# Performance work log

Hardware: AMD Instinct MI355X
Metric: run time of the kernel (lower is better)

Reference implementation:

```python
import jax, jax.numpy as jnp
import numpy as np

EPS = 1e-5  # batch-norm epsilon


def subm_conv(feat, nbrs, W):
    # feat: [N, Cin], nbrs: [N, K] int indices into feat (rulebook), W: [K, Cin, Cout]
    gathered = feat[nbrs]                      # [N, K, Cin]  irregular gather
    return jnp.einsum('nkc,kcd->nd', gathered, W)


def batch_norm(f, gamma, beta):
    # training-mode BN over active sites (scn.BatchNormalization semantics)
    mean = jnp.mean(f, axis=0)
    var = jnp.var(f, axis=0)
    return (f - mean) * jax.lax.rsqrt(var + EPS) * gamma + beta


def setup_inputs() -> dict:
    key = jax.random.key(0)
    k1, k2, k3, k4 = jax.random.split(key, 4)
    N, K, C = 300000, 9, 64
    scale = 1.0 / np.sqrt(K * C)
    return {
        'x': jax.random.normal(k1, (N, C), dtype=jnp.float32),
        'nbrs': jax.random.randint(k2, (N, K), 0, N, dtype=jnp.int32),
        'W1': jax.random.normal(k3, (K, C, C), dtype=jnp.float32) * scale,
        'gamma1': jnp.ones((C,), jnp.float32),
        'beta1': jnp.zeros((C,), jnp.float32),
        'W2': jax.random.normal(k4, (K, C, C), dtype=jnp.float32) * scale,
        'gamma2': jnp.ones((C,), jnp.float32),
        'beta2': jnp.zeros((C,), jnp.float32),
    }


def reference(x, nbrs, W1, gamma1, beta1, W2, gamma2, beta2):
    residual = x
    out = subm_conv(x, nbrs, W1)                       # conv1 (no bias)
    out = jax.nn.relu(batch_norm(out, gamma1, beta1))  # BatchNormReLU
    out = subm_conv(out, nbrs, W2)                     # conv2 (no bias)
    out = batch_norm(out, gamma2, beta2)               # BatchNormalization
    out = jax.nn.relu(out + residual)                  # AddTable + ReLU
    return out
```

## Files before the change

### kernel.cpp

```cpp
#include <hip/hip_runtime.h>

#define NROWS 300000
#define NBLK ((NROWS + 63) / 64)

typedef float f32x4 __attribute__((ext_vector_type(4)));
typedef short s16x8 __attribute__((ext_vector_type(8)));
typedef unsigned short u16x8 __attribute__((ext_vector_type(8)));
typedef unsigned short u16x4 __attribute__((ext_vector_type(4)));

__device__ __forceinline__ float bf2f(unsigned short u) {
    return __uint_as_float(((unsigned)u) << 16);
}
__device__ __forceinline__ unsigned short f2bf(float f) {
    unsigned u = __float_as_uint(f);
    u += 0x7FFFu + ((u >> 16) & 1u);
    return (unsigned short)(u >> 16);
}

__global__ __launch_bounds__(256) void x2bf(const float* __restrict__ x,
                                            unsigned short* __restrict__ xb) {
    const int NQ = NROWS * 8;
    for (int i = blockIdx.x * 256 + threadIdx.x; i < NQ; i += gridDim.x * 256) {
        const float4 v0 = *(const float4*)(x + (size_t)i * 8);
        const float4 v1 = *(const float4*)(x + (size_t)i * 8 + 4);
        u16x8 o;
        o[0] = f2bf(v0.x); o[1] = f2bf(v0.y); o[2] = f2bf(v0.z); o[3] = f2bf(v0.w);
        o[4] = f2bf(v1.x); o[5] = f2bf(v1.y); o[6] = f2bf(v1.z); o[7] = f2bf(v1.w);
        *(u16x8*)(xb + (size_t)i * 8) = o;
    }
}

__global__ __launch_bounds__(256) void w_prep(const float* __restrict__ W1,
                                              const float* __restrict__ W2,
                                              unsigned short* __restrict__ WT1,
                                              unsigned short* __restrict__ WT2) {
    const int i = blockIdx.x * 256 + threadIdx.x;
    if (i < 9 * 4096) {
        const int k = i >> 12, cc = (i >> 6) & 63, d = i & 63;
        const int o = k * 4096 + d * 64 + cc;
        WT1[o] = f2bf(W1[i]);
        WT2[o] = f2bf(W2[i]);
    }
}

__global__ __launch_bounds__(256) void conv_mfma(const unsigned short* __restrict__ xb,
                                                 const int* __restrict__ nbrs,
                                                 const unsigned short* __restrict__ WT,
                                                 unsigned short* __restrict__ outb) {
    const int tid = threadIdx.x;
    const int l = tid & 63;
    const int w = tid >> 6;
    const int lr = l & 15;
    const int kg = l >> 4;
    const int c00 = kg * 8;

    const int rowA = blockIdx.x * 64 + w * 16 + lr;
    const int rowAc = rowA < NROWS ? rowA : NROWS - 1;

    int nb[9];
#pragma unroll
    for (int k = 0; k < 9; ++k) nb[k] = nbrs[rowAc * 9 + k];

    s16x8 raw0[9], raw1[9];
#pragma unroll
    for (int k = 0; k < 9; ++k) {
        const unsigned short* rp = xb + (size_t)nb[k] * 64 + c00;
        asm volatile("global_load_dwordx4 %0, %1, off"
                     : "=v"(raw0[k]) : "v"(rp));
        asm volatile("global_load_dwordx4 %0, %1, off offset:64"
                     : "=v"(raw1[k]) : "v"(rp));
    }
    asm volatile("s_waitcnt vmcnt(0)" ::: "memory");
    __builtin_amdgcn_sched_barrier(0);

    f32x4 acc[4];
#pragma unroll
    for (int d = 0; d < 4; ++d) {
        acc[d][0] = 0.f; acc[d][1] = 0.f; acc[d][2] = 0.f; acc[d][3] = 0.f;
    }

#pragma unroll
    for (int k = 0; k < 9; ++k) {
        const unsigned short* wp = WT + k * 4096 + lr * 64 + c00;
#pragma unroll
        for (int dj = 0; dj < 4; ++dj) {
            const s16x8 b0 = *(const s16x8*)(wp + dj * 1024);
            const s16x8 b1 = *(const s16x8*)(wp + dj * 1024 + 32);
            acc[dj] = __builtin_amdgcn_mfma_f32_16x16x32_bf16(raw0[k], b0, acc[dj], 0, 0, 0);
            acc[dj] = __builtin_amdgcn_mfma_f32_16x16x32_bf16(raw1[k], b1, acc[dj], 0, 0, 0);
        }
    }

    const int orow0 = blockIdx.x * 64 + w * 16 + kg * 4;
#pragma unroll
    for (int dj = 0; dj < 4; ++dj) {
#pragma unroll
        for (int r = 0; r < 4; ++r) {
            const int orow = orow0 + r;
            if (orow < NROWS) outb[(size_t)orow * 64 + dj * 16 + lr] = f2bf(acc[dj][r]);
        }
    }
}

__global__ __launch_bounds__(256) void bn_stats(const unsigned short* __restrict__ fb,
                                                float* __restrict__ S) {
    const int t = threadIdx.x;
    const int c4 = (t & 15) * 4;
    const int rg = t >> 4;
    float s0 = 0, s1 = 0, s2 = 0, s3 = 0, q0 = 0, q1 = 0, q2 = 0, q3 = 0;
    for (int r = blockIdx.x * 16 + rg; r < NROWS; r += gridDim.x * 16) {
        const u16x4 v = *(const u16x4*)(fb + (size_t)r * 64 + c4);
        const float f0 = bf2f(v[0]), f1 = bf2f(v[1]), f2 = bf2f(v[2]), f3 = bf2f(v[3]);
        s0 += f0; s1 += f1; s2 += f2; s3 += f3;
        q0 += f0 * f0; q1 += f1 * f1; q2 += f2 * f2; q3 += f3 * f3;
    }
    __shared__ float red[16][64];
    red[rg][c4 + 0] = s0; red[rg][c4 + 1] = s1; red[rg][c4 + 2] = s2; red[rg][c4 + 3] = s3;
    __syncthreads();
    if (t < 64) {
        float a = 0;
#pragma unroll
        for (int i = 0; i < 16; ++i) a += red[i][t];
        atomicAdd(&S[t], a);
    }
    __syncthreads();
    red[rg][c4 + 0] = q0; red[rg][c4 + 1] = q1; red[rg][c4 + 2] = q2; red[rg][c4 + 3] = q3;
    __syncthreads();
    if (t < 64) {
        float a = 0;
#pragma unroll
        for (int i = 0; i < 16; ++i) a += red[i][t];
        atomicAdd(&S[64 + t], a);
    }
}

__global__ void bn_finalize(const float* __restrict__ S, const float* __restrict__ gamma,
                            const float* __restrict__ beta, float* __restrict__ sb) {
    const int c = threadIdx.x;
    if (c < 64) {
        const float mean = S[c] * (1.0f / NROWS);
        const float var = S[64 + c] * (1.0f / NROWS) - mean * mean;
        const float sc = gamma[c] * rsqrtf(var + 1e-5f);
        sb[c] = sc;
        sb[64 + c] = beta[c] - mean * sc;
    }
}

__global__ __launch_bounds__(256) void bn_apply(unsigned short* __restrict__ fb,
                                                const float* __restrict__ sb) {
    const int NQ = NROWS * 8;
    for (int i = blockIdx.x * 256 + threadIdx.x; i < NQ; i += gridDim.x * 256) {
        const int c8 = (i & 7) * 8;
        u16x8 v = *(const u16x8*)(fb + (size_t)i * 8);
        u16x8 o;
#pragma unroll
        for (int j = 0; j < 8; ++j) {
            const float f = fmaxf(bf2f(v[j]) * sb[c8 + j] + sb[64 + c8 + j], 0.f);
            o[j] = f2bf(f);
        }
        *(u16x8*)(fb + (size_t)i * 8) = o;
    }
}

__global__ __launch_bounds__(256) void final_out(const unsigned short* __restrict__ o2,
                                                 const float* __restrict__ x,
                                                 const float* __restrict__ sb,
                                                 float* __restrict__ out) {
    const int NQ = NROWS * 16;
    for (int i = blockIdx.x * 256 + threadIdx.x; i < NQ; i += gridDim.x * 256) {
        const int c4 = (i & 15) * 4;
        const u16x4 v = *(const u16x4*)(o2 + (size_t)i * 4);
        const float4 xv = *(const float4*)(x + (size_t)i * 4);
        const float4 s = *(const float4*)(sb + c4);
        const float4 b = *(const float4*)(sb + 64 + c4);
        float4 o;
        o.x = fmaxf(bf2f(v[0]) * s.x + b.x + xv.x, 0.f);
        o.y = fmaxf(bf2f(v[1]) * s.y + b.y + xv.y, 0.f);
        o.z = fmaxf(bf2f(v[2]) * s.z + b.z + xv.z, 0.f);
        o.w = fmaxf(bf2f(v[3]) * s.w + b.w + xv.w, 0.f);
        *(float4*)(out + (size_t)i * 4) = o;
    }
}

extern "C" void kernel_launch(void* const* d_in, const int* in_sizes, int n_in,
                              void* d_out, int out_size, void* d_ws, size_t ws_size,
                              hipStream_t stream) {
    const float* x      = (const float*)d_in[0];
    const int*   nbrs   = (const int*)d_in[1];
    const float* W1     = (const float*)d_in[2];
    const float* gamma1 = (const float*)d_in[3];
    const float* beta1  = (const float*)d_in[4];
    const float* W2     = (const float*)d_in[5];
    const float* gamma2 = (const float*)d_in[6];
    const float* beta2  = (const float*)d_in[7];
    float* out = (float*)d_out;

    char* ws = (char*)d_ws;
    unsigned short* out2b = (unsigned short*)ws;
    unsigned short* WT1   = (unsigned short*)(ws + 38400000);
    unsigned short* WT2   = (unsigned short*)(ws + 38400000 + 73728);
    float* Sa  = (float*)(ws + 38400000 + 147456);
    float* Sb  = Sa + 128;
    float* sb1 = Sa + 256;
    float* sb2 = Sa + 384;
    unsigned short* out1b = (unsigned short*)d_out;
    unsigned short* xb    = (unsigned short*)d_out + 19200000;

    hipMemsetAsync(Sa, 0, 256 * sizeof(float), stream);
    x2bf<<<2048, 256, 0, stream>>>(x, xb);
    w_prep<<<144, 256, 0, stream>>>(W1, W2, WT1, WT2);
    conv_mfma<<<NBLK, 256, 0, stream>>>(xb, nbrs, WT1, out1b);
    bn_stats<<<1024, 256, 0, stream>>>(out1b, Sa);
    bn_finalize<<<1, 64, 0, stream>>>(Sa, gamma1, beta1, sb1);
    bn_apply<<<2048, 256, 0, stream>>>(out1b, sb1);
    conv_mfma<<<NBLK, 256, 0, stream>>>(out1b, nbrs, WT2, out2b);
    bn_stats<<<1024, 256, 0, stream>>>(out2b, Sb);
    bn_finalize<<<1, 64, 0, stream>>>(Sb, gamma2, beta2, sb2);
    final_out<<<2048, 256, 0, stream>>>(out2b, x, sb2, out);
}
```

Before: 530.7 us.

## Gather neighbor rows directly into LDS with swizzled global_load_lds

Replaces the per-lane register gathers of neighbor feature rows with global_load_lds transfers into a per-wave LDS buffer. Each group of 8 lanes fetches one full 128-byte row, with an XOR swizzle on the 16-byte chunk index. The MFMA A operands are then read back from LDS using the matching swizzle. The aim is fully coalesced row-sized gathers and lower VGPR pressure, at the cost of 72KB of LDS per block, which limits occupancy, plus extra LDS reads.

New measurement: 527.7 us. Within noise of the previous version (-0.6%).

```diff
diff --git a/kernel.cpp b/kernel.cpp
--- a/kernel.cpp
+++ b/kernel.cpp
@@ -15,6 +15,12 @@
     unsigned u = __float_as_uint(f);
     u += 0x7FFFu + ((u >> 16) & 1u);
     return (unsigned short)(u >> 16);
+}
+
+__device__ __forceinline__ void load_lds16(const void* g, void* lds) {
+    __builtin_amdgcn_global_load_lds(
+        (const __attribute__((address_space(1))) void*)g,
+        (__attribute__((address_space(3))) void*)lds, 16, 0, 0);
 }
 
 __global__ __launch_bounds__(256) void x2bf(const float* __restrict__ x,
@@ -47,6 +53,8 @@
                                                  const int* __restrict__ nbrs,
                                                  const unsigned short* __restrict__ WT,
                                                  unsigned short* __restrict__ outb) {
+    __shared__ __align__(1024) char lds_raw[4 * 18432];
+
     const int tid = threadIdx.x;
     const int l = tid & 63;
     const int w = tid >> 6;
@@ -54,21 +62,26 @@
     const int kg = l >> 4;
     const int c00 = kg * 8;
 
-    const int rowA = blockIdx.x * 64 + w * 16 + lr;
-    const int rowAc = rowA < NROWS ? rowA : NROWS - 1;
-
-    int nb[9];
-#pragma unroll
-    for (int k = 0; k < 9; ++k) nb[k] = nbrs[rowAc * 9 + k];
-
-    s16x8 raw0[9], raw1[9];
+    const int rowbase = blockIdx.x * 64 + w * 16;
+
+    const int rsub = l >> 3;
+    const int b16 = ((l & 7) ^ rsub) << 4;
+    const int rA = min(rowbase + rsub, NROWS - 1);
+    const int rB = min(rowbase + 8 + rsub, NROWS - 1);
+
+    int nbA[9], nbB[9];
 #pragma unroll
     for (int k = 0; k < 9; ++k) {
-        const unsigned short* rp = xb + (size_t)nb[k] * 64 + c00;
-        asm volatile("global_load_dwordx4 %0, %1, off"
-                     : "=v"(raw0[k]) : "v"(rp));
-        asm volatile("global_load_dwordx4 %0, %1, off offset:64"
-                     : "=v"(raw1[k]) : "v"(rp));
+        nbA[k] = nbrs[rA * 9 + k];
+        nbB[k] = nbrs[rB * 9 + k];
+    }
+
+    char* wbase = lds_raw + w * 18432;
+    const char* xbc = (const char*)xb;
+#pragma unroll
+    for (int k = 0; k < 9; ++k) {
+        load_lds16(xbc + (size_t)nbA[k] * 128 + b16, wbase + k * 2048);
+        load_lds16(xbc + (size_t)nbB[k] * 128 + b16, wbase + k * 2048 + 1024);
     }
     asm volatile("s_waitcnt vmcnt(0)" ::: "memory");
     __builtin_amdgcn_sched_barrier(0);
@@ -79,19 +92,23 @@
         acc[d][0] = 0.f; acc[d][1] = 0.f; acc[d][2] = 0.f; acc[d][3] = 0.f;
     }
 
+    const int swz = (lr & 7) << 4;
 #pragma unroll
     for (int k = 0; k < 9; ++k) {
+        const char* tk = wbase + k * 2048 + lr * 128;
+        const s16x8 a0 = *(const s16x8*)(tk + ((c00 * 2) ^ swz));
+        const s16x8 a1 = *(const s16x8*)(tk + ((64 + c00 * 2) ^ swz));
         const unsigned short* wp = WT + k * 4096 + lr * 64 + c00;
 #pragma unroll
         for (int dj = 0; dj < 4; ++dj) {
             const s16x8 b0 = *(const s16x8*)(wp + dj * 1024);
             const s16x8 b1 = *(const s16x8*)(wp + dj * 1024 + 32);
-            acc[dj] = __builtin_amdgcn_mfma_f32_16x16x32_bf16(raw0[k], b0, acc[dj], 0, 0, 0);
-            acc[dj] = __builtin_amdgcn_mfma_f32_16x16x32_bf16(raw1[k], b1, acc[dj], 0, 0, 0);
+            acc[dj] = __builtin_amdgcn_mfma_f32_16x16x32_bf16(a0, b0, acc[dj], 0, 0, 0);
+            acc[dj] = __builtin_amdgcn_mfma_f32_16x16x32_bf16(a1, b1, acc[dj], 0, 0, 0);
         }
     }
 
-    const int orow0 = blockIdx.x * 64 + w * 16 + kg * 4;
+    const int orow0 = rowbase + kg * 4;
 #pragma unroll
     for (int dj = 0; dj < 4; ++dj) {
 #pragma unroll
```
